# Kernel optimization log

Measured on AMD Instinct MI355X. Metric: run time of the kernel, lower is better.

Reference implementation:

```python
import jax, jax.numpy as jnp
import numpy as np

N, E, IN_DIM, OUT_DIM, NTYPE, QDIM = 32, 512, 300, 300, 4, 300
SLOPE = 0.2  # lrelu:0.2


def setup_inputs() -> dict:
    key = jax.random.key(0)
    ks = jax.random.split(key, 8)
    return {
        "input_state": jax.random.normal(ks[0], (N, E, IN_DIM), jnp.float32),
        "adj": jax.random.randint(ks[1], (N, E, E), 0, NTYPE + 1, dtype=jnp.int32),
        "node_mask": jax.random.uniform(ks[2], (N, E, 1), jnp.float32),
        "query_vec": jax.random.normal(ks[3], (N, QDIM), jnp.float32),
        "W_type": jax.random.normal(ks[4], (NTYPE, IN_DIM, OUT_DIM), jnp.float32) * 0.02,
        "a_type": jax.random.normal(ks[5], (NTYPE, 2 * OUT_DIM), jnp.float32) * 0.02,
        "qattn_W1": jax.random.normal(ks[6], (NTYPE, QDIM, 2 * OUT_DIM), jnp.float32) * 0.02,
        "qattn_W2": jax.random.normal(ks[7], (NTYPE, 2 * OUT_DIM, 2 * OUT_DIM), jnp.float32) * 0.02,
    }


def reference(input_state, adj, node_mask, query_vec, W_type, a_type, qattn_W1, qattn_W2):
    # Faithful GAT head. The original builds an [N,E,E,2d] concat tensor; since
    # a_input[n,i,j] = [h_i, h_j] and the gate broadcasts over (i,j), the score
    # decomposes exactly as lrelu((h*g1)@a1 [:,i,None] + (h*g2)@a2 [:,None,j]).
    lrelu = lambda x: jnp.where(x >= 0, x, SLOPE * x)
    scores = jnp.zeros(adj.shape, jnp.float32)
    h = None
    for i in range(NTYPE):
        h = jnp.einsum("ned,df->nef", input_state, W_type[i])  # [N,E,d] (dropout: eval no-op)
        q_gate = jax.nn.relu(query_vec @ qattn_W1[i])
        q_gate = jax.nn.sigmoid(q_gate @ qattn_W2[i])          # [N,2d]
        g1, g2 = q_gate[:, :OUT_DIM], q_gate[:, OUT_DIM:]
        a1, a2 = a_type[i][:OUT_DIM], a_type[i][OUT_DIM:]
        s_src = jnp.einsum("ned,d->ne", h * g1[:, None, :], a1)  # contributes along i
        s_dst = jnp.einsum("ned,d->ne", h * g2[:, None, :], a2)  # contributes along j
        score = lrelu(s_src[:, :, None] + s_dst[:, None, :])      # [N,E,E]
        scores = scores + jnp.where(adj == i + 1, score, 0.0)
    scores = jnp.where(adj > 0, scores, jnp.float32(-1e30))
    h = h * node_mask  # note: original applies mask to h from the LAST edge type
    coefs = jax.nn.softmax(scores, axis=2)
    return jnp.einsum("nij,njd->nid", coefs, h)
```

## Files before the change

kernel.cpp:

```cpp
#include <hip/hip_runtime.h>
#include <hip/hip_bf16.h>

#define Nn   32
#define Ee   512
#define DIN  300
#define DOUT 300
#define NT   4
#define QD   300
#define SLOPE 0.2f
#define ROWS 32
#define CPAD 320

typedef __attribute__((ext_vector_type(8))) short bf16x8;
typedef __attribute__((ext_vector_type(4))) float f32x4;
typedef __attribute__((ext_vector_type(4))) unsigned short u16x4;

__device__ inline unsigned short f2bf(float x) {
    __hip_bfloat16 h = __float2bfloat16(x);
    return *reinterpret_cast<unsigned short*>(&h);
}
__device__ inline float bf2f(unsigned short u) {
    __hip_bfloat16 h = *reinterpret_cast<__hip_bfloat16*>(&u);
    return __bfloat162float(h);
}

__global__ __launch_bounds__(256) void prep_kernel(
    const float* __restrict__ W3,
    unsigned short* __restrict__ W3T_hi,
    unsigned short* __restrict__ W3T_lo,
    unsigned short* __restrict__ UTh,
    unsigned short* __restrict__ UTl,
    unsigned short* __restrict__ GTh,
    unsigned short* __restrict__ GTl)
{
    int idx = blockIdx.x * 256 + threadIdx.x;
    if (idx < 320 * 320) {
        int c = idx / 320, k = idx - c * 320;
        float v = (c < DOUT && k < DIN) ? W3[(size_t)k * DOUT + c] : 0.f;
        unsigned short h = f2bf(v);
        W3T_hi[idx] = h;
        W3T_lo[idx] = f2bf(v - bf2f(h));
    }
    if (idx < 32 * 16 * 320) { UTh[idx] = 0; UTl[idx] = 0; }
    if (idx < 4 * 64 * 320)  { GTh[idx] = 0; GTl[idx] = 0; }
}

__global__ __launch_bounds__(256) void gates1_part_kernel(
    const float* __restrict__ q,
    const float* __restrict__ W1,
    float* __restrict__ t1p)
{
    int i = blockIdx.y, z = blockIdx.z;
    int idx = blockIdx.x * 256 + threadIdx.x;
    int n = idx / 600, j = idx - n * 600;
    const float* W1i = W1 + (size_t)i * QD * 600;
    const float* qn = q + n * QD;
    int k0 = z * 75;
    float a0 = 0.f;
    #pragma unroll 5
    for (int k = k0; k < k0 + 75; ++k)
        a0 += qn[k] * W1i[(size_t)k * 600 + j];
    t1p[((size_t)(z * NT + i) * Nn + n) * 600 + j] = a0;
}

__global__ __launch_bounds__(256) void gates1_fin_kernel(
    const float* __restrict__ t1p, float* __restrict__ t1)
{
    int i = blockIdx.y;
    int idx = blockIdx.x * 256 + threadIdx.x;
    size_t o = ((size_t)i * Nn) * 600 + idx;
    float s = t1p[o] + t1p[o + 76800] + t1p[o + 2 * 76800] + t1p[o + 3 * 76800];
    t1[o] = fmaxf(s, 0.f);
}

__global__ __launch_bounds__(256) void gates2_part_kernel(
    const float* __restrict__ t1,
    const float* __restrict__ W2,
    float* __restrict__ gp)
{
    int i = blockIdx.y, z = blockIdx.z;
    int idx = blockIdx.x * 256 + threadIdx.x;
    int n = idx / 600, j = idx - n * 600;
    const float* W2i = W2 + (size_t)i * 600 * 600;
    const float* tn = t1 + ((size_t)i * Nn + n) * 600;
    int k0 = z * 150;
    float a0 = 0.f, a1 = 0.f;
    #pragma unroll 5
    for (int k = k0; k < k0 + 150; k += 2) {
        a0 += tn[k]     * W2i[(size_t)k * 600 + j];
        a1 += tn[k + 1] * W2i[(size_t)(k + 1) * 600 + j];
    }
    gp[((size_t)(z * NT + i) * Nn + n) * 600 + j] = a0 + a1;
}

__global__ __launch_bounds__(256) void gates2_fin_kernel(
    const float* __restrict__ gp,
    const float* __restrict__ a,
    unsigned short* __restrict__ GTh,
    unsigned short* __restrict__ GTl)
{
    int i = blockIdx.y;
    int idx = blockIdx.x * 256 + threadIdx.x;
    int n = idx / 600, j = idx - n * 600;
    size_t o = ((size_t)i * Nn + n) * 600 + j;
    float s = gp[o] + gp[o + 76800] + gp[o + 2 * 76800] + gp[o + 3 * 76800];
    float w = (1.f / (1.f + __expf(-s))) * a[(size_t)i * 600 + j];
    int s2 = (j >= DOUT) ? 1 : 0;
    int d = j - s2 * DOUT;
    int c = 2 * n + s2;
    size_t go = ((size_t)i * 64 + c) * 320 + d;
    unsigned short h = f2bf(w);
    GTh[go] = h;
    GTl[go] = f2bf(w - bf2f(h));
}

__global__ __launch_bounds__(256) void uvec_mfma_kernel(
    const float* __restrict__ W,
    const unsigned short* __restrict__ GTh,
    const unsigned short* __restrict__ GTl,
    unsigned short* __restrict__ UTh,
    unsigned short* __restrict__ UTl)
{
    int mc = blockIdx.x, i = blockIdx.y;
    int tid = threadIdx.x, wv = tid >> 6, lane = tid & 63;
    int g = lane >> 4, cr = lane & 15;
    int m0 = mc * 64 + wv * 16;
    int arow = m0 + cr;
    const float* wr = W + (size_t)i * DIN * DOUT
                        + (size_t)(arow < DIN ? arow : 0) * DOUT;

    f32x4 acc[4];
    #pragma unroll
    for (int nt = 0; nt < 4; ++nt) acc[nt] = (f32x4){0.f, 0.f, 0.f, 0.f};

    for (int ks = 0; ks < 10; ++ks) {
        int k0 = ks * 32 + 8 * g;
        float x8[8];
        if (ks < 9) {
            f32x4 v0 = *(const f32x4*)(wr + k0);
            f32x4 v1 = *(const f32x4*)(wr + k0 + 4);
            #pragma unroll
            for (int j = 0; j < 4; ++j) { x8[j] = v0[j]; x8[4 + j] = v1[j]; }
        } else {
            #pragma unroll
            for (int j = 0; j < 8; ++j) {
                int d = k0 + j;
                x8[j] = (d < DOUT) ? wr[d] : 0.f;
            }
        }
        bf16x8 ahi, alo;
        #pragma unroll
        for (int j = 0; j < 8; ++j) {
            unsigned short h = f2bf(x8[j]);
            ahi[j] = (short)h;
            alo[j] = (short)f2bf(x8[j] - bf2f(h));
        }
        #pragma unroll
        for (int nt = 0; nt < 4; ++nt) {
            size_t bo = ((size_t)i * 64 + nt * 16 + cr) * 320 + k0;
            bf16x8 bh = *(const bf16x8*)(GTh + bo);
            bf16x8 bl = *(const bf16x8*)(GTl + bo);
            acc[nt] = __builtin_amdgcn_mfma_f32_16x16x32_bf16(ahi, bh, acc[nt], 0, 0, 0);
            acc[nt] = __builtin_amdgcn_mfma_f32_16x16x32_bf16(ahi, bl, acc[nt], 0, 0, 0);
            acc[nt] = __builtin_amdgcn_mfma_f32_16x16x32_bf16(alo, bh, acc[nt], 0, 0, 0);
        }
    }

    int krow = m0 + 4 * g;
    if (krow < DIN) {
        #pragma unroll
        for (int nt = 0; nt < 4; ++nt) {
            int c = nt * 16 + cr;
            int n = c >> 1, s = c & 1;
            size_t base = ((size_t)n * 16 + 2 * i + s) * 320 + krow;
            u16x4 h4, l4;
            #pragma unroll
            for (int q = 0; q < 4; ++q) {
                float v = acc[nt][q];
                unsigned short h = f2bf(v);
                h4[q] = h;
                l4[q] = f2bf(v - bf2f(h));
            }
            *(u16x4*)(UTh + base) = h4;
            *(u16x4*)(UTl + base) = l4;
        }
    }
}

__global__ __launch_bounds__(256) void hm_mfma_kernel(
    const float* __restrict__ X,
    const float* __restrict__ mask,
    const unsigned short* __restrict__ W3T_hi,
    const unsigned short* __restrict__ W3T_lo,
    const unsigned short* __restrict__ UTh,
    const unsigned short* __restrict__ UTl,
    unsigned short* __restrict__ hmT_hi,
    unsigned short* __restrict__ hmT_lo,
    float* __restrict__ ssrc,
    float* __restrict__ sdst)
{
    int tid = threadIdx.x, wv = tid >> 6, lane = tid & 63;
    int g = lane >> 4, cr = lane & 15;
    size_t row0 = (size_t)blockIdx.x * 32;
    int n = (int)(row0 >> 9), j0 = (int)(row0 & 511);

    __shared__ float maskL[32];
    if (tid < 32) maskL[tid] = mask[row0 + tid];
    __syncthreads();

    f32x4 acc[5][2];
    f32x4 sacc[2];
    #pragma unroll
    for (int a = 0; a < 5; ++a)
        #pragma unroll
        for (int m = 0; m < 2; ++m) acc[a][m] = (f32x4){0.f, 0.f, 0.f, 0.f};
    sacc[0] = (f32x4){0.f, 0.f, 0.f, 0.f};
    sacc[1] = (f32x4){0.f, 0.f, 0.f, 0.f};

    const float* xr0 = X + (row0 + cr) * DIN;
    const float* xr1 = X + (row0 + 16 + cr) * DIN;

    for (int ks = 0; ks < 10; ++ks) {
        int k0 = ks * 32 + 8 * g;
        bf16x8 ahi[2], alo[2];
        #pragma unroll
        for (int m = 0; m < 2; ++m) {
            const float* xr = m ? xr1 : xr0;
            float x8[8];
            if (ks < 9) {
                f32x4 v0 = *(const f32x4*)(xr + k0);
                f32x4 v1 = *(const f32x4*)(xr + k0 + 4);
                #pragma unroll
                for (int j = 0; j < 4; ++j) { x8[j] = v0[j]; x8[4 + j] = v1[j]; }
            } else {
                #pragma unroll
                for (int j = 0; j < 8; ++j) {
                    int k = k0 + j;
                    x8[j] = (k < DIN) ? xr[k] : 0.f;
                }
            }
            #pragma unroll
            for (int j = 0; j < 8; ++j) {
                unsigned short h = f2bf(x8[j]);
                ahi[m][j] = (short)h;
                alo[m][j] = (short)f2bf(x8[j] - bf2f(h));
            }
        }
        #pragma unroll
        for (int ntl = 0; ntl < 5; ++ntl) {
            int c = (wv + 4 * ntl) * 16 + cr;
            bf16x8 bh = *(const bf16x8*)(W3T_hi + (size_t)c * 320 + k0);
            bf16x8 bl = *(const bf16x8*)(W3T_lo + (size_t)c * 320 + k0);
            #pragma unroll
            for (int m = 0; m < 2; ++m) {
                acc[ntl][m] = __builtin_amdgcn_mfma_f32_16x16x32_bf16(ahi[m], bh, acc[ntl][m], 0, 0, 0);
                acc[ntl][m] = __builtin_amdgcn_mfma_f32_16x16x32_bf16(ahi[m], bl, acc[ntl][m], 0, 0, 0);
                acc[ntl][m] = __builtin_amdgcn_mfma_f32_16x16x32_bf16(alo[m], bh, acc[ntl][m], 0, 0, 0);
            }
        }
        if (wv == 0) {
            bf16x8 uh = *(const bf16x8*)(UTh + ((size_t)n * 16 + cr) * 320 + k0);
            bf16x8 ul = *(const bf16x8*)(UTl + ((size_t)n * 16 + cr) * 320 + k0);
            #pragma unroll
            for (int m = 0; m < 2; ++m) {
                sacc[m] = __builtin_amdgcn_mfma_f32_16x16x32_bf16(ahi[m], uh, sacc[m], 0, 0, 0);
                sacc[m] = __builtin_amdgcn_mfma_f32_16x16x32_bf16(ahi[m], ul, sacc[m], 0, 0, 0);
                sacc[m] = __builtin_amdgcn_mfma_f32_16x16x32_bf16(alo[m], uh, sacc[m], 0, 0, 0);
            }
        }
    }

    #pragma unroll
    for (int ntl = 0; ntl < 5; ++ntl) {
        int c = (wv + 4 * ntl) * 16 + cr;
        #pragma unroll
        for (int m = 0; m < 2; ++m) {
            u16x4 h4, l4;
            #pragma unroll
            for (int qq = 0; qq < 4; ++qq) {
                float v = acc[ntl][m][qq] * maskL[m * 16 + 4 * g + qq];
                unsigned short h = f2bf(v);
                h4[qq] = h;
                l4[qq] = f2bf(v - bf2f(h));
            }
            size_t off = ((size_t)(n * CPAD + c)) * Ee + j0 + m * 16 + 4 * g;
            *(u16x4*)(hmT_hi + off) = h4;
            *(u16x4*)(hmT_lo + off) = l4;
        }
    }

    if (wv == 0 && cr < 8) {
        int i = cr >> 1;
        float* dst = (cr & 1) ? sdst : ssrc;
        #pragma unroll
        for (int m = 0; m < 2; ++m)
            #pragma unroll
            for (int qq = 0; qq < 4; ++qq)
                dst[((size_t)i * Nn + n) * Ee + j0 + m * 16 + 4 * g + qq] = sacc[m][qq];
    }
}

__global__ __launch_bounds__(512, 4) void attn8_kernel(
    const int*   __restrict__ adj,
    const float* __restrict__ ssrc,
    const float* __restrict__ sdst,
    const unsigned short* __restrict__ hmT_hi,
    const unsigned short* __restrict__ hmT_lo,
    float* __restrict__ out)
{
    int f  = blockIdx.x;
    int n  = (f & 7) * 4 + ((f >> 3) & 3);
    int rt = f >> 5;
    int tid = threadIdx.x;
    int row0 = rt * ROWS;

    __shared__ unsigned coefT[Ee * 33];
    __shared__ float sdl[NT * Ee];
    __shared__ float ssl[NT * ROWS];

    for (int idx = tid; idx < NT * Ee; idx += 512) {
        int i = idx >> 9, j = idx & (Ee - 1);
        sdl[idx] = sdst[((size_t)i * Nn + n) * Ee + j];
    }
    for (int idx = tid; idx < NT * ROWS; idx += 512) {
        int i = idx >> 5, r = idx & 31;
        ssl[idx] = ssrc[((size_t)i * Nn + n) * Ee + row0 + r];
    }
    __syncthreads();

    const int* adjb = adj + ((size_t)n * Ee + row0) * Ee;
    for (int idx4 = tid; idx4 < (ROWS * Ee) / 4; idx4 += 512) {
        int r  = idx4 >> 7;
        int jb = (idx4 & 127) << 2;
        int4 t4 = *(const int4*)(adjb + (idx4 << 2));
        int tv[4] = {t4.x, t4.y, t4.z, t4.w};
        #pragma unroll
        for (int u = 0; u < 4; ++u) {
            int t = tv[u];
            int j = jb + u;
            float v;
            if (t > 0) {
                float x = ssl[(t - 1) * ROWS + r] + sdl[(t - 1) * Ee + j];
                v = (x >= 0.f) ? x : SLOPE * x;
            } else {
                v = -1e30f;
            }
            coefT[j * 33 + r] = __float_as_uint(v);
        }
    }
    __syncthreads();

    int wv = tid >> 6, lane = tid & 63;
    #pragma unroll
    for (int rr = 0; rr < 4; ++rr) {
        int r = wv * 4 + rr;
        float vals[8];
        float m = -3.0e38f;
        #pragma unroll
        for (int k = 0; k < 8; ++k) {
            vals[k] = __uint_as_float(coefT[(lane + 64 * k) * 33 + r]);
            m = fmaxf(m, vals[k]);
        }
        #pragma unroll
        for (int off = 32; off; off >>= 1) m = fmaxf(m, __shfl_xor(m, off));
        float s = 0.f;
        #pragma unroll
        for (int k = 0; k < 8; ++k) {
            vals[k] = __expf(vals[k] - m);
            s += vals[k];
        }
        #pragma unroll
        for (int off = 32; off; off >>= 1) s += __shfl_xor(s, off);
        float inv = 1.f / s;
        #pragma unroll
        for (int k = 0; k < 8; ++k)
            coefT[(lane + 64 * k) * 33 + r] = __float_as_uint(vals[k] * inv);
    }
    __syncthreads();

    for (int idx = tid; idx < Ee * ROWS; idx += 512) {
        int j = idx >> 5, r = idx & 31;
        float v = __uint_as_float(coefT[j * 33 + r]);
        unsigned short hi = f2bf(v);
        unsigned short lo = f2bf(v - bf2f(hi));
        coefT[j * 33 + r] = ((unsigned)hi << 16) | (unsigned)lo;
    }
    __syncthreads();

    int g = lane >> 4, cr = lane & 15;
    f32x4 acc[3][2];
    #pragma unroll
    for (int t = 0; t < 3; ++t)
        #pragma unroll
        for (int m = 0; m < 2; ++m) acc[t][m] = (f32x4){0.f, 0.f, 0.f, 0.f};

#define LOADB(BH, BL, KS) do {                                              \
    int kk_ = (KS) * 32 + 8 * g;                                            \
    _Pragma("unroll")                                                       \
    for (int t_ = 0; t_ < 3; ++t_) {                                        \
        int ct_ = wv + 8 * t_;                                              \
        if (ct_ < 20) {                                                     \
            size_t off_ = ((size_t)(n * CPAD + ct_ * 16 + cr)) * Ee + kk_;  \
            BH[t_] = *(const bf16x8*)(hmT_hi + off_);                       \
            BL[t_] = *(const bf16x8*)(hmT_lo + off_);                       \
        }                                                                   \
    }                                                                       \
} while (0)

#define PVSTEP(KS, BH, BL) do {                                             \
    int kk_ = (KS) * 32;                                                    \
    bf16x8 ahi_[2], alo_[2];                                                \
    _Pragma("unroll")                                                       \
    for (int m_ = 0; m_ < 2; ++m_) {                                        \
        _Pragma("unroll")                                                   \
        for (int j_ = 0; j_ < 8; ++j_) {                                    \
            unsigned v_ = coefT[(kk_ + 8 * g + j_) * 33 + m_ * 16 + cr];    \
            ahi_[m_][j_] = (short)(v_ >> 16);                               \
            alo_[m_][j_] = (short)(v_ & 0xffffu);                           \
        }                                                                   \
    }                                                                       \
    __builtin_amdgcn_s_setprio(1);                                          \
    _Pragma("unroll")                                                       \
    for (int t_ = 0; t_ < 3; ++t_) {                                        \
        if (wv + 8 * t_ < 20) {                                             \
            _Pragma("unroll")                                               \
            for (int m_ = 0; m_ < 2; ++m_) {                                \
                acc[t_][m_] = __builtin_amdgcn_mfma_f32_16x16x32_bf16(ahi_[m_], BH[t_], acc[t_][m_], 0, 0, 0); \
                acc[t_][m_] = __builtin_amdgcn_mfma_f32_16x16x32_bf16(ahi_[m_], BL[t_], acc[t_][m_], 0, 0, 0); \
                acc[t_][m_] = __builtin_amdgcn_mfma_f32_16x16x32_bf16(alo_[m_], BH[t_], acc[t_][m_], 0, 0, 0); \
            }                                                               \
        }                                                                   \
    }                                                                       \
    __builtin_amdgcn_s_setprio(0);                                          \
} while (0)

    bf16x8 bhA[3], blA[3], bhB[3], blB[3];
    LOADB(bhA, blA, 0);
    #pragma unroll
    for (int ks = 0; ks < 16; ks += 2) {
        LOADB(bhB, blB, ks + 1);
        PVSTEP(ks, bhA, blA);
        if (ks + 2 < 16) LOADB(bhA, blA, ks + 2);
        PVSTEP(ks + 1, bhB, blB);
    }
#undef LOADB
#undef PVSTEP

    #pragma unroll
    for (int t = 0; t < 3; ++t) {
        int ct = wv + 8 * t;
        if (ct < 20) {
            int c = ct * 16 + cr;
            if (c < DOUT) {
                #pragma unroll
                for (int m = 0; m < 2; ++m) {
                    #pragma unroll
                    for (int q = 0; q < 4; ++q) {
                        int erow = row0 + m * 16 + 4 * g + q;
                        out[((size_t)n * Ee + erow) * DOUT + c] = acc[t][m][q];
                    }
                }
            }
        }
    }
}

extern "C" void kernel_launch(void* const* d_in, const int* in_sizes, int n_in,
                              void* d_out, int out_size, void* d_ws, size_t ws_size,
                              hipStream_t stream) {
    const float* input_state = (const float*)d_in[0];
    const int*   adj         = (const int*)  d_in[1];
    const float* node_mask   = (const float*)d_in[2];
    const float* query_vec   = (const float*)d_in[3];
    const float* W_type      = (const float*)d_in[4];
    const float* a_type      = (const float*)d_in[5];
    const float* qattn_W1    = (const float*)d_in[6];
    const float* qattn_W2    = (const float*)d_in[7];
    float* out = (float*)d_out;

    float* ws   = (float*)d_ws;
    float* t1   = ws;
    float* ssrc = t1   + 76800;
    float* sdst = ssrc + 65536;
    unsigned short* W3T_hi = (unsigned short*)(sdst + 65536);
    unsigned short* W3T_lo = W3T_hi + 320 * 320;
    unsigned short* GTh    = W3T_lo + 320 * 320;
    unsigned short* GTl    = GTh + 4 * 64 * 320;
    unsigned short* UTh    = GTl + 4 * 64 * 320;
    unsigned short* UTl    = UTh + 32 * 16 * 320;
    unsigned short* hmT_hi = UTl + 32 * 16 * 320;
    unsigned short* hmT_lo = hmT_hi + (size_t)Nn * CPAD * Ee;
    float* t1p = (float*)(hmT_lo + (size_t)Nn * CPAD * Ee);
    float* gp  = t1p + 307200;

    hipLaunchKernelGGL(prep_kernel, dim3(640), dim3(256), 0, stream,
                       W_type + 3 * DIN * DOUT, W3T_hi, W3T_lo, UTh, UTl, GTh, GTl);
    hipLaunchKernelGGL(gates1_part_kernel, dim3(75, NT, 4), dim3(256), 0, stream,
                       query_vec, qattn_W1, t1p);
    hipLaunchKernelGGL(gates1_fin_kernel, dim3(75, NT), dim3(256), 0, stream,
                       t1p, t1);
    hipLaunchKernelGGL(gates2_part_kernel, dim3(75, NT, 4), dim3(256), 0, stream,
                       t1, qattn_W2, gp);
    hipLaunchKernelGGL(gates2_fin_kernel, dim3(75, NT), dim3(256), 0, stream,
                       gp, a_type, GTh, GTl);
    hipLaunchKernelGGL(uvec_mfma_kernel, dim3(5, NT), dim3(256), 0, stream,
                       W_type, GTh, GTl, UTh, UTl);
    hipLaunchKernelGGL(hm_mfma_kernel, dim3((Nn * Ee) / 32), dim3(256), 0, stream,
                       input_state, node_mask, W3T_hi, W3T_lo, UTh, UTl,
                       hmT_hi, hmT_lo, ssrc, sdst);
    hipLaunchKernelGGL(attn8_kernel, dim3(512), dim3(512), 0, stream,
                       adj, ssrc, sdst, hmT_hi, hmT_lo, out);
}
```

Baseline: 142.4 us.

## Double attention row tile to 64 and keep softmax values in registers

The attention kernel now handles 64 query rows per block instead of 32 and runs on half as many blocks, so each bf16 hi/lo B fragment of h loaded from global memory feeds twice as many MFMAs. Scores are written row-major with vector stores. Softmax values stay in registers and are normalised and split into bf16 hi/lo in one pass, which removes an extra LDS round trip. The cost is about 142KB of LDS per block and one block per CU, which leaves less latency hiding and more register pressure.

```diff
diff --git a/kernel.cpp b/kernel.cpp
--- a/kernel.cpp
+++ b/kernel.cpp
@@ -8,8 +8,10 @@
 #define NT   4
 #define QD   300
 #define SLOPE 0.2f
-#define ROWS 32
+#define ROWS 64
 #define CPAD 320
+#define SSTR 516
+#define USTR 65
 
 typedef __attribute__((ext_vector_type(8))) short bf16x8;
 typedef __attribute__((ext_vector_type(4))) float f32x4;
@@ -300,7 +302,7 @@
     }
 }
 
-__global__ __launch_bounds__(512, 4) void attn8_kernel(
+__global__ __launch_bounds__(512, 1) void attn64_kernel(
     const int*   __restrict__ adj,
     const float* __restrict__ ssrc,
     const float* __restrict__ sdst,
@@ -314,17 +316,18 @@
     int tid = threadIdx.x;
     int row0 = rt * ROWS;
 
-    __shared__ unsigned coefT[Ee * 33];
+    __shared__ unsigned uni[Ee * USTR];
     __shared__ float sdl[NT * Ee];
-    __shared__ float ssl[NT * ROWS];
+    __shared__ float ssl[NT * 65];
+    float* S = (float*)uni;
 
     for (int idx = tid; idx < NT * Ee; idx += 512) {
         int i = idx >> 9, j = idx & (Ee - 1);
         sdl[idx] = sdst[((size_t)i * Nn + n) * Ee + j];
     }
-    for (int idx = tid; idx < NT * ROWS; idx += 512) {
-        int i = idx >> 5, r = idx & 31;
-        ssl[idx] = ssrc[((size_t)i * Nn + n) * Ee + row0 + r];
+    if (tid < NT * ROWS) {
+        int i = tid >> 6, r = tid & 63;
+        ssl[i * 65 + r] = ssrc[((size_t)i * Nn + n) * Ee + row0 + r];
     }
     __syncthreads();
 
@@ -334,65 +337,69 @@
         int jb = (idx4 & 127) << 2;
         int4 t4 = *(const int4*)(adjb + (idx4 << 2));
         int tv[4] = {t4.x, t4.y, t4.z, t4.w};
+        f32x4 v4;
         #pragma unroll
         for (int u = 0; u < 4; ++u) {
             int t = tv[u];
             int j = jb + u;
             float v;
             if (t > 0) {
-                float x = ssl[(t - 1) * ROWS + r] + sdl[(t - 1) * Ee + j];
+                float x = ssl[(t - 1) * 65 + r] + sdl[(t - 1) * Ee + j];
                 v = (x >= 0.f) ? x : SLOPE * x;
             } else {
                 v = -1e30f;
             }
-            coefT[j * 33 + r] = __float_as_uint(v);
-        }
+            v4[u] = v;
+        }
+        *(f32x4*)(S + r * SSTR + jb) = v4;
     }
     __syncthreads();
 
     int wv = tid >> 6, lane = tid & 63;
-    #pragma unroll
-    for (int rr = 0; rr < 4; ++rr) {
-        int r = wv * 4 + rr;
-        float vals[8];
+    float vals[8][8];
+    float inv[8];
+    #pragma unroll
+    for (int rr = 0; rr < 8; ++rr) {
+        int r = wv * 8 + rr;
         float m = -3.0e38f;
         #pragma unroll
         for (int k = 0; k < 8; ++k) {
-            vals[k] = __uint_as_float(coefT[(lane + 64 * k) * 33 + r]);
-            m = fmaxf(m, vals[k]);
+            vals[rr][k] = S[r * SSTR + lane + 64 * k];
+            m = fmaxf(m, vals[rr][k]);
         }
         #pragma unroll
         for (int off = 32; off; off >>= 1) m = fmaxf(m, __shfl_xor(m, off));
         float s = 0.f;
         #pragma unroll
         for (int k = 0; k < 8; ++k) {
-            vals[k] = __expf(vals[k] - m);
-            s += vals[k];
+            vals[rr][k] = __expf(vals[rr][k] - m);
+            s += vals[rr][k];
         }
         #pragma unroll
         for (int off = 32; off; off >>= 1) s += __shfl_xor(s, off);
-        float inv = 1.f / s;
-        #pragma unroll
-        for (int k = 0; k < 8; ++k)
-            coefT[(lane + 64 * k) * 33 + r] = __float_as_uint(vals[k] * inv);
+        inv[rr] = 1.f / s;
     }
     __syncthreads();
 
-    for (int idx = tid; idx < Ee * ROWS; idx += 512) {
-        int j = idx >> 5, r = idx & 31;
-        float v = __uint_as_float(coefT[j * 33 + r]);
-        unsigned short hi = f2bf(v);
-        unsigned short lo = f2bf(v - bf2f(hi));
-        coefT[j * 33 + r] = ((unsigned)hi << 16) | (unsigned)lo;
+    #pragma unroll
+    for (int rr = 0; rr < 8; ++rr) {
+        int r = wv * 8 + rr;
+        #pragma unroll
+        for (int k = 0; k < 8; ++k) {
+            float v = vals[rr][k] * inv[rr];
+            unsigned short hi = f2bf(v);
+            unsigned short lo = f2bf(v - bf2f(hi));
+            uni[(lane + 64 * k) * USTR + r] = ((unsigned)hi << 16) | (unsigned)lo;
+        }
     }
     __syncthreads();
 
     int g = lane >> 4, cr = lane & 15;
-    f32x4 acc[3][2];
+    f32x4 acc[3][4];
     #pragma unroll
     for (int t = 0; t < 3; ++t)
         #pragma unroll
-        for (int m = 0; m < 2; ++m) acc[t][m] = (f32x4){0.f, 0.f, 0.f, 0.f};
+        for (int m = 0; m < 4; ++m) acc[t][m] = (f32x4){0.f, 0.f, 0.f, 0.f};
 
 #define LOADB(BH, BL, KS) do {                                              \
     int kk_ = (KS) * 32 + 8 * g;                                            \
@@ -409,12 +416,12 @@
 
 #define PVSTEP(KS, BH, BL) do {                                             \
     int kk_ = (KS) * 32;                                                    \
-    bf16x8 ahi_[2], alo_[2];                                                \
+    bf16x8 ahi_[4], alo_[4];                                                \
     _Pragma("unroll")                                                       \
-    for (int m_ = 0; m_ < 2; ++m_) {                                        \
+    for (int m_ = 0; m_ < 4; ++m_) {                                        \
         _Pragma("unroll")                                                   \
         for (int j_ = 0; j_ < 8; ++j_) {                                    \
-            unsigned v_ = coefT[(kk_ + 8 * g + j_) * 33 + m_ * 16 + cr];    \
+            unsigned v_ = uni[(kk_ + 8 * g + j_) * USTR + m_ * 16 + cr];    \
             ahi_[m_][j_] = (short)(v_ >> 16);                               \
             alo_[m_][j_] = (short)(v_ & 0xffffu);                           \
         }                                                                   \
@@ -424,7 +431,7 @@
     for (int t_ = 0; t_ < 3; ++t_) {                                        \
         if (wv + 8 * t_ < 20) {                                             \
             _Pragma("unroll")                                               \
-            for (int m_ = 0; m_ < 2; ++m_) {                                \
+            for (int m_ = 0; m_ < 4; ++m_) {                                \
                 acc[t_][m_] = __builtin_amdgcn_mfma_f32_16x16x32_bf16(ahi_[m_], BH[t_], acc[t_][m_], 0, 0, 0); \
                 acc[t_][m_] = __builtin_amdgcn_mfma_f32_16x16x32_bf16(ahi_[m_], BL[t_], acc[t_][m_], 0, 0, 0); \
                 acc[t_][m_] = __builtin_amdgcn_mfma_f32_16x16x32_bf16(alo_[m_], BH[t_], acc[t_][m_], 0, 0, 0); \
@@ -453,7 +460,7 @@
             int c = ct * 16 + cr;
             if (c < DOUT) {
                 #pragma unroll
-                for (int m = 0; m < 2; ++m) {
+                for (int m = 0; m < 4; ++m) {
                     #pragma unroll
                     for (int q = 0; q < 4; ++q) {
                         int erow = row0 + m * 16 + 4 * g + q;
@@ -508,6 +515,6 @@
     hipLaunchKernelGGL(hm_mfma_kernel, dim3((Nn * Ee) / 32), dim3(256), 0, stream,
                        input_state, node_mask, W3T_hi, W3T_lo, UTh, UTl,
                        hmT_hi, hmT_lo, ssrc, sdst);
-    hipLaunchKernelGGL(attn8_kernel, dim3(512), dim3(512), 0, stream,
+    hipLaunchKernelGGL(attn64_kernel, dim3(256), dim3(512), 0, stream,
                        adj, ssrc, sdst, hmT_hi, hmT_lo, out);
 }
```

Result: faster. 129.9 us (-8.8%).
